# Kernel optimization log

Measured on AMD Instinct MI355X. Metric: run time of the kernel, lower is better.

## Reference

```python
import jax, jax.numpy as jnp
import numpy as np

FOCUS = 3  # focusing_factor
EPS = 1e-6


def setup_inputs() -> dict:
    key = jax.random.key(0)
    ks = jax.random.split(key, 6)
    B, N, C = 4, 4096, 1024
    s = 0.02
    return {
        "x": jax.random.normal(ks[0], (B, N, C), jnp.float32),
        "w_qkv": jax.random.normal(ks[1], (3 * C, C), jnp.float32) * s,
        "w_proj": jax.random.normal(ks[2], (C, C), jnp.float32) * s,
        "b_proj": jax.random.normal(ks[3], (C,), jnp.float32) * s,
        "w_dwc": jax.random.normal(ks[4], (C, 3), jnp.float32) * s,
        "b_dwc": jax.random.normal(ks[5], (C,), jnp.float32) * s,
    }


def _norm_last(t):
    return t / jnp.sum(t, axis=-1, keepdims=True)


def reference(x, w_qkv, w_proj, b_proj, w_dwc, b_dwc):
    B, N, C = x.shape
    H = 16
    d = C // H
    # qkv projection -> (3, B, H, N, d)
    qkv = jnp.einsum('bnc,oc->bno', x, w_qkv).reshape(B, N, 3, H, d)
    qkv = jnp.transpose(qkv, (2, 0, 3, 1, 4))
    q, k, v = qkv[0], qkv[1], qkv[2]
    # focused kernel feature map: relu -> l1 norm -> power -> renorm
    q = _norm_last(jax.nn.relu(q) + EPS)
    k = _norm_last(jax.nn.relu(k) + EPS)
    q = _norm_last(q ** FOCUS)
    k = _norm_last(k ** FOCUS)
    # linear attention
    kv = jnp.einsum('bhnd,bhne->bhde', k, v)                     # (B,H,d,d)
    z = 1.0 / (jnp.einsum('bhnd,bhd->bhn', q, k.sum(axis=2)) + EPS)
    out = jnp.einsum('bhnd,bhde,bhn->bhne', q, kv, z)            # (B,H,N,d)
    out = jnp.transpose(out, (0, 2, 1, 3)).reshape(B, N, C)
    # depthwise conv1d over sequence, kernel=3, padding=1 (torch layout [C,1,3])
    xp = jnp.pad(out, ((0, 0), (1, 1), (0, 0)))
    conv = (xp[:, 0:N, :] * w_dwc[:, 0]
            + xp[:, 1:N + 1, :] * w_dwc[:, 1]
            + xp[:, 2:N + 2, :] * w_dwc[:, 2]) + b_dwc
    out = out + conv
    # output projection (dropout is identity in eval)
    return jnp.einsum('bnc,oc->bno', out, w_proj) + b_proj
```

## Files before the change

kernel.cpp:

```cpp
#include <hip/hip_runtime.h>
#include <hip/hip_bf16.h>

#define BB 4
#define NN 4096
#define CC 1024
#define HH 16
#define MM (BB*NN)
#define EPSF 1e-6f

typedef _Float16 f16x8 __attribute__((ext_vector_type(8)));
typedef float f32x4 __attribute__((ext_vector_type(4)));

__device__ __forceinline__ void gload_lds16(const void* g, void* l) {
    __builtin_amdgcn_global_load_lds(
        (const __attribute__((address_space(1))) void*)g,
        (__attribute__((address_space(3))) void*)l, 16, 0, 0);
}

__device__ __forceinline__ float h2f(short s) {
    return (float)__builtin_bit_cast(_Float16, s);
}

__global__ __launch_bounds__(256)
void tofp16_kernel(const float* __restrict__ src, _Float16* __restrict__ dst, int n4)
{
    int i = blockIdx.x * 256 + threadIdx.x;
    if (i < n4) {
        float4 f = ((const float4*)src)[i];
        short4 pk;
        pk.x = __builtin_bit_cast(short, (_Float16)f.x);
        pk.y = __builtin_bit_cast(short, (_Float16)f.y);
        pk.z = __builtin_bit_cast(short, (_Float16)f.z);
        pk.w = __builtin_bit_cast(short, (_Float16)f.w);
        ((short4*)dst)[i] = pk;
    }
}


#define STAGE(BUF, KT) do {                                                          \
    _Pragma("unroll")                                                                \
    for (int j_ = 0; j_ < 2; ++j_) {                                                 \
        gload_lds16(gA[j_] + (KT) * 32, (char*)lds + (BUF) * 32768 + lbase[j_]);     \
        gload_lds16(gB[j_] + (KT) * 32, (char*)lds + (BUF) * 32768 + 16384 + lbase[j_]); \
    } } while (0)

#define TILE(KT, CUR, NXT, DOSTAGE, VMSTR) do {                                      \
    if (DOSTAGE) STAGE(NXT, (KT) + 2);                                               \
    const char* Ab_ = (const char*)lds + (CUR) * 32768 + aoff;                       \
    const char* Bb_ = (const char*)lds + (CUR) * 32768 + 16384 + boff;               \
    f16x8 af_[8], bf_[4];                                                            \
    _Pragma("unroll")                                                                \
    for (int m_ = 0; m_ < 8; ++m_) af_[m_] = *(const f16x8*)(Ab_ + m_ * 1024);       \
    _Pragma("unroll")                                                                \
    for (int n_ = 0; n_ < 4; ++n_) bf_[n_] = *(const f16x8*)(Bb_ + n_ * 1024);       \
    __builtin_amdgcn_s_setprio(1);                                                   \
    _Pragma("unroll")                                                                \
    for (int m_ = 0; m_ < 8; ++m_)                                                   \
    _Pragma("unroll")                                                                \
    for (int n_ = 0; n_ < 4; ++n_)                                                   \
        acc[m_][n_] = __builtin_amdgcn_mfma_f32_16x16x32_f16(af_[m_], bf_[n_],       \
                                                             acc[m_][n_], 0, 0, 0); \
    __builtin_amdgcn_s_setprio(0);                                                   \
    asm volatile("s_waitcnt " VMSTR ::: "memory");                                   \
    __builtin_amdgcn_s_barrier();                                                    \
    __builtin_amdgcn_sched_barrier(0);                                               \
} while (0)

template<int EPI>
__global__ __launch_bounds__(512, 2)
void gemm256(const _Float16* __restrict__ A, const _Float16* __restrict__ Bm,
             void* __restrict__ Cout, _Float16* __restrict__ Kt,
             _Float16* __restrict__ Vt, const float* __restrict__ bias,
             const int Ncols, const int gx)
{
    __shared__ _Float16 lds[3 * 16384];

    const int tid  = threadIdx.x;
    const int lane = tid & 63;
    const int wid  = tid >> 6;
    const int wm   = wid >> 2;
    const int wn   = wid & 3;

    const int nwg = gridDim.x;
    const int wg  = blockIdx.x;
    const int sw  = (wg & 7) * (nwg >> 3) + (wg >> 3);
    const int by  = sw / gx, bx = sw - by * gx;
    const int brow = by << 8, bcol = bx << 8;

    const _Float16* gA[2]; const _Float16* gB[2]; int lbase[2];
#pragma unroll
    for (int j = 0; j < 2; ++j) {
        int pos = ((wid * 2 + j) << 10) + (lane << 4);
        int r   = pos >> 6;
        int c8  = ((pos >> 4) & 3) ^ ((r >> 1) & 3);
        gA[j] = A  + (size_t)(brow + r) * 1024 + c8 * 8;
        gB[j] = Bm + (size_t)(bcol + r) * 1024 + c8 * 8;
        lbase[j] = (wid * 2 + j) << 10;
    }

    const int swz  = (((lane >> 4) ^ ((lane >> 1) & 3)) << 4);
    const int aoff = (wm * 128 + (lane & 15)) * 64 + swz;
    const int boff = (wn * 64  + (lane & 15)) * 64 + swz;

    f32x4 acc[8][4] = {};

    STAGE(0, 0);
    STAGE(1, 1);
    asm volatile("s_waitcnt vmcnt(4)" ::: "memory");
    __builtin_amdgcn_s_barrier();
    __builtin_amdgcn_sched_barrier(0);

#pragma unroll 1
    for (int tt = 0; tt < 30; tt += 3) {
        TILE(tt,     0, 2, 1, "vmcnt(4)");
        TILE(tt + 1, 1, 0, 1, "vmcnt(4)");
        TILE(tt + 2, 2, 1, 1, "vmcnt(4)");
    }
    TILE(30, 0, 2, 0, "vmcnt(0)");
    TILE(31, 1, 0, 0, "vmcnt(0)");

    if (EPI == 0) {
        const int sec = bcol >> 10;
        const bool feat = (sec < 2);
        if (feat) {
#pragma unroll
            for (int m = 0; m < 8; ++m)
#pragma unroll
                for (int r = 0; r < 4; ++r) {
                    float u[4]; float ssum = 0.f;
#pragma unroll
                    for (int n = 0; n < 4; ++n) {
                        float uu = fmaxf(acc[m][n][r], 0.f) + EPSF;
                        float c = uu * uu * uu;
                        u[n] = c; ssum += c;
                    }
                    ssum += __shfl_xor(ssum, 1, 16);
                    ssum += __shfl_xor(ssum, 2, 16);
                    ssum += __shfl_xor(ssum, 4, 16);
                    ssum += __shfl_xor(ssum, 8, 16);
                    float inv = 1.0f / ssum;
#pragma unroll
                    for (int n = 0; n < 4; ++n) acc[m][n][r] = u[n] * inv;
                }
        }
        if (sec == 0) {
            _Float16* Fo = (_Float16*)Cout;
            const int colb = bcol + wn * 64 + (lane & 15);
#pragma unroll
            for (int m = 0; m < 8; ++m) {
                int rb = brow + wm * 128 + m * 16 + (lane >> 4) * 4;
#pragma unroll
                for (int r = 0; r < 4; ++r) {
                    size_t base = (size_t)(rb + r) * 1024 + colb;
#pragma unroll
                    for (int n = 0; n < 4; ++n)
                        Fo[base + n * 16] = (_Float16)acc[m][n][r];
                }
            }
        } else {
            _Float16* T = (sec == 1) ? Kt : Vt;
            const int b   = brow >> 12;
            const int hb  = ((bcol & 1023) >> 6) + wn;
            const int bh  = b * 16 + hb;
            const int n0  = (brow & 4095) + wm * 128;
            char* st = (char*)lds + wid * 8704;
            const int p = lane & 15, q2 = lane >> 4;
#pragma unroll
            for (int c2 = 0; c2 < 2; ++c2) {
#pragma unroll
                for (int m = 0; m < 4; ++m) {
                    int mm = c2 * 4 + m;
                    int tokc = m * 16 + q2 * 4;
#pragma unroll
                    for (int n = 0; n < 4; ++n) {
                        short4 pk;
                        pk.x = __builtin_bit_cast(short, (_Float16)acc[mm][n][0]);
                        pk.y = __builtin_bit_cast(short, (_Float16)acc[mm][n][1]);
                        pk.z = __builtin_bit_cast(short, (_Float16)acc[mm][n][2]);
                        pk.w = __builtin_bit_cast(short, (_Float16)acc[mm][n][3]);
                        int dk = n * 16 + p;
                        *(short4*)(st + dk * 136 + tokc * 2) = pk;
                    }
                }
#pragma unroll
                for (int it = 0; it < 16; ++it) {
                    int dk = it * 4 + q2;
                    short4 v4 = *(const short4*)(st + dk * 136 + p * 8);
                    *(short4*)(T + ((size_t)(bh * 64 + dk)) * 4096 + n0 + c2 * 64 + p * 4) = v4;
                }
            }
        }
    } else {
        float* Oc = (float*)Cout;
        const int colb = bcol + wn * 64 + (lane & 15);
#pragma unroll
        for (int m = 0; m < 8; ++m) {
            int rb = brow + wm * 128 + m * 16 + (lane >> 4) * 4;
#pragma unroll
            for (int r = 0; r < 4; ++r) {
                size_t base = (size_t)(rb + r) * Ncols + colb;
#pragma unroll
                for (int n = 0; n < 4; ++n)
                    Oc[base + n * 16] = acc[m][n][r] + bias[colb + n * 16];
            }
        }
    }
}

__global__ __launch_bounds__(256)
void kv_mfma(const _Float16* __restrict__ Kt, const _Float16* __restrict__ Vt,
             float* __restrict__ kvp, float* __restrict__ ksump)
{
    __shared__ float red[4][64][64];
    __shared__ float ksr[4][64];
    int bx = blockIdx.x;
    int bh = bx >> 2, kseg = bx & 3;
    int tid = threadIdx.x;
    int w = tid >> 6, lane = tid & 63, p = lane & 15, q = lane >> 4;
    const _Float16* Vb = Vt + (size_t)bh * 64 * 4096;
    const _Float16* Kb = Kt + (size_t)bh * 64 * 4096;
    f32x4 acc[4][4] = {};
    float ksp[4] = {0.f, 0.f, 0.f, 0.f};
    int kbase = kseg * 1024 + w * 256 + q * 8;
#pragma unroll 1
    for (int ks = 0; ks < 8; ++ks) {
        int kb = kbase + ks * 32;
        f16x8 af[4], bf[4];
#pragma unroll
        for (int m = 0; m < 4; ++m)
            af[m] = *(const f16x8*)(Vb + (size_t)(m * 16 + p) * 4096 + kb);
#pragma unroll
        for (int n = 0; n < 4; ++n) {
            bf[n] = *(const f16x8*)(Kb + (size_t)(n * 16 + p) * 4096 + kb);
#pragma unroll
            for (int j = 0; j < 8; ++j) ksp[n] += (float)bf[n][j];
        }
#pragma unroll
        for (int m = 0; m < 4; ++m)
#pragma unroll
            for (int n = 0; n < 4; ++n)
                acc[m][n] = __builtin_amdgcn_mfma_f32_16x16x32_f16(
                    af[m], bf[n], acc[m][n], 0, 0, 0);
    }
#pragma unroll
    for (int n = 0; n < 4; ++n) {
        ksp[n] += __shfl_xor(ksp[n], 16);
        ksp[n] += __shfl_xor(ksp[n], 32);
    }
    if (q == 0)
#pragma unroll
        for (int n = 0; n < 4; ++n) ksr[w][n * 16 + p] = ksp[n];
#pragma unroll
    for (int m = 0; m < 4; ++m)
#pragma unroll
        for (int n = 0; n < 4; ++n)
            *(f32x4*)&red[w][n * 16 + p][m * 16 + q * 4] = acc[m][n];
    __syncthreads();
    int dv = tid & 63, dkb = (tid >> 6) * 16;
    float* ko = kvp + ((size_t)(kseg * 64 + bh)) * 4096;
    f32x4 o[4];
#pragma unroll
    for (int i = 0; i < 16; ++i) {
        float s = red[0][dkb + i][dv] + red[1][dkb + i][dv]
                + red[2][dkb + i][dv] + red[3][dkb + i][dv];
        o[i >> 2][i & 3] = s;
    }
#pragma unroll
    for (int i = 0; i < 4; ++i)
        *(f32x4*)(ko + dv * 64 + dkb + i * 4) = o[i];
    if (tid < 64)
        ksump[(size_t)(kseg * 64 + bh) * 64 + tid] =
            ksr[0][tid] + ksr[1][tid] + ksr[2][tid] + ksr[3][tid];
}

__global__ __launch_bounds__(256)
void kv_reduce(const float* __restrict__ kvp, const float* __restrict__ ksump,
               _Float16* __restrict__ kvT, float* __restrict__ ksum)
{
    int idx = blockIdx.x * 256 + threadIdx.x;
    float s = kvp[idx] + kvp[262144 + idx] + kvp[2 * 262144 + idx] + kvp[3 * 262144 + idx];
    kvT[idx] = (_Float16)s;
    if (idx < 4096)
        ksum[idx] = ksump[idx] + ksump[4096 + idx] + ksump[2 * 4096 + idx] + ksump[3 * 4096 + idx];
}

__global__ __launch_bounds__(256)
void attn_conv(const _Float16* __restrict__ Fq, const _Float16* __restrict__ kvT,
               const float* __restrict__ ksum, const float* __restrict__ wdwc,
               const float* __restrict__ bdwc, _Float16* __restrict__ yf)
{
    __shared__ _Float16 ybuf[258][68];
    __shared__ float kslds[64];
    int blk = blockIdx.x;
    int b = blk >> 8, h = (blk >> 4) & 15, chunk = blk & 15;
    int bh = b * 16 + h;
    int tid = threadIdx.x, w = tid >> 6, lane = tid & 63, p = lane & 15, q = lane >> 4;
    if (tid < 64) kslds[tid] = ksum[bh * 64 + tid];
    const _Float16* kvb = kvT + (size_t)bh * 4096;
    f16x8 bf[2][4];
#pragma unroll
    for (int kst = 0; kst < 2; ++kst)
#pragma unroll
        for (int n = 0; n < 4; ++n)
            bf[kst][n] = *(const f16x8*)(kvb + (n * 16 + p) * 64 + kst * 32 + q * 8);
    __syncthreads();

    int tok0 = chunk * 256 + w * 64;
    const size_t rowbase = (size_t)(b * 4096 + tok0);
    f16x8 qr[8];
#pragma unroll
    for (int i = 0; i < 8; ++i)
        qr[i] = *(const f16x8*)(Fq + (rowbase + lane) * 1024 + h * 64 + i * 8);
    float s = 0.f;
#pragma unroll
    for (int i = 0; i < 8; ++i)
#pragma unroll
        for (int j = 0; j < 8; ++j)
            s += (float)qr[i][j] * kslds[i * 8 + j];
    float z = 1.0f / (s + EPSF);

    f32x4 acc[4][4] = {};
#pragma unroll
    for (int kst = 0; kst < 2; ++kst) {
        f16x8 af[4];
#pragma unroll
        for (int m = 0; m < 4; ++m)
            af[m] = *(const f16x8*)(Fq + (rowbase + m * 16 + p) * 1024 + h * 64 + kst * 32 + q * 8);
#pragma unroll
        for (int m = 0; m < 4; ++m)
#pragma unroll
            for (int n = 0; n < 4; ++n)
                acc[m][n] = __builtin_amdgcn_mfma_f32_16x16x32_f16(
                    af[m], bf[kst][n], acc[m][n], 0, 0, 0);
    }
#pragma unroll
    for (int m = 0; m < 4; ++m)
#pragma unroll
        for (int r = 0; r < 4; ++r) {
            float zz = __shfl(z, m * 16 + q * 4 + r);
            int row = 1 + w * 64 + m * 16 + q * 4 + r;
#pragma unroll
            for (int n = 0; n < 4; ++n)
                ybuf[row][n * 16 + p] = (_Float16)(acc[m][n][r] * zz);
        }
    if (w == 0) {
        float val = 0.f;
        if (chunk > 0) {
            int t = chunk * 256 - 1;
            float sd = 0.f, sz = 0.f;
#pragma unroll
            for (int i = 0; i < 8; ++i) {
                f16x8 qq = *(const f16x8*)(Fq + ((size_t)(b * 4096 + t)) * 1024 + h * 64 + i * 8);
                f16x8 kk = *(const f16x8*)(kvb + lane * 64 + i * 8);
#pragma unroll
                for (int j = 0; j < 8; ++j) {
                    sd += (float)qq[j] * (float)kk[j];
                    sz += (float)qq[j] * kslds[i * 8 + j];
                }
            }
            val = sd / (sz + EPSF);
        }
        ybuf[0][lane] = (_Float16)val;
    }
    if (w == 3) {
        float val = 0.f;
        if (chunk < 15) {
            int t = chunk * 256 + 256;
            float sd = 0.f, sz = 0.f;
#pragma unroll
            for (int i = 0; i < 8; ++i) {
                f16x8 qq = *(const f16x8*)(Fq + ((size_t)(b * 4096 + t)) * 1024 + h * 64 + i * 8);
                f16x8 kk = *(const f16x8*)(kvb + lane * 64 + i * 8);
#pragma unroll
                for (int j = 0; j < 8; ++j) {
                    sd += (float)qq[j] * (float)kk[j];
                    sz += (float)qq[j] * kslds[i * 8 + j];
                }
            }
            val = sd / (sz + EPSF);
        }
        ybuf[257][lane] = (_Float16)val;
    }
    __syncthreads();
    int dv = lane;
    int c = h * 64 + dv;
    float w0 = wdwc[c * 3 + 0], w1 = wdwc[c * 3 + 1], w2 = wdwc[c * 3 + 2];
    float bb = bdwc[c];
#pragma unroll 4
    for (int it = 0; it < 64; ++it) {
        int tok = it * 4 + w;
        float ym = (float)ybuf[tok][dv];
        float yc = (float)ybuf[tok + 1][dv];
        float yp = (float)ybuf[tok + 2][dv];
        float val = yc + w0 * ym + w1 * yc + w2 * yp + bb;
        yf[((size_t)(b * 4096 + chunk * 256 + tok)) * 1024 + c] = (_Float16)val;
    }
}

extern "C" void kernel_launch(void* const* d_in, const int* in_sizes, int n_in,
                              void* d_out, int out_size, void* d_ws, size_t ws_size,
                              hipStream_t stream)
{
    const float* x      = (const float*)d_in[0];
    const float* w_qkv  = (const float*)d_in[1];
    const float* w_proj = (const float*)d_in[2];
    const float* b_proj = (const float*)d_in[3];
    const float* w_dwc  = (const float*)d_in[4];
    const float* b_dwc  = (const float*)d_in[5];

    char* p = (char*)d_ws;
    _Float16* xf   = (_Float16*)p;  p += (size_t)MM * CC * 2;
    _Float16* wqf  = (_Float16*)p;  p += (size_t)3 * CC * CC * 2;
    _Float16* wpf  = (_Float16*)p;  p += (size_t)CC * CC * 2;
    _Float16* Fq   = (_Float16*)p;  p += (size_t)MM * CC * 2;
    _Float16* Kt   = (_Float16*)p;  p += (size_t)64 * 64 * NN * 2;
    _Float16* Vt   = (_Float16*)p;  p += (size_t)64 * 64 * NN * 2;
    float*    kvp  = (float*)p;     p += (size_t)4 * 64 * 4096 * 4;
    float*    ksump= (float*)p;     p += (size_t)4 * 64 * 64 * 4;
    _Float16* kvT  = (_Float16*)p;  p += (size_t)64 * 4096 * 2;
    float*    ksum = (float*)p;     p += (size_t)64 * 64 * 4;
    _Float16* yf   = (_Float16*)p;  p += (size_t)MM * CC * 2;

    tofp16_kernel<<<(MM * CC / 4 + 255) / 256, 256, 0, stream>>>(x, xf, MM * CC / 4);
    tofp16_kernel<<<(3 * CC * CC / 4 + 255) / 256, 256, 0, stream>>>(w_qkv, wqf, 3 * CC * CC / 4);
    tofp16_kernel<<<(CC * CC / 4 + 255) / 256, 256, 0, stream>>>(w_proj, wpf, CC * CC / 4);

    gemm256<0><<<dim3(12 * 64), 512, 0, stream>>>(
        xf, wqf, (void*)Fq, Kt, Vt, nullptr, 3072, 12);

    kv_mfma<<<256, 256, 0, stream>>>(Kt, Vt, kvp, ksump);
    kv_reduce<<<1024, 256, 0, stream>>>(kvp, ksump, kvT, ksum);

    attn_conv<<<BB * HH * 16, 256, 0, stream>>>(Fq, kvT, ksum, w_dwc, b_dwc, yf);

    gemm256<1><<<dim3(4 * 64), 512, 0, stream>>>(
        yf, wpf, d_out, nullptr, nullptr, b_proj, 1024, 4);
}
```

Before: 224.2 us.

## Restructure GEMM main loop to K=64 double-buffered tiles with interleaved staging

The 256x256 fp16 GEMM main loop moves from a triple-buffered K=32 pipeline to a double-buffered K=64 tile with a new XOR swizzle for 128-byte rows. Each tile is split into four MFMA phases with barriers, and the global-to-LDS loads for the next tile are interleaved between phases. The goal is to halve loop iterations and barrier overhead per K step and to overlap LDS fragment reads and global loads with MFMA work. In exchange it needs more LDS (128KB per block, which may cut occupancy below the launch bound of 2) and adds more barriers within each tile.

```diff
diff --git a/kernel.cpp b/kernel.cpp
--- a/kernel.cpp
+++ b/kernel.cpp
@@ -37,34 +37,85 @@
 }
 
 
-#define STAGE(BUF, KT) do {                                                          \
-    _Pragma("unroll")                                                                \
-    for (int j_ = 0; j_ < 2; ++j_) {                                                 \
-        gload_lds16(gA[j_] + (KT) * 32, (char*)lds + (BUF) * 32768 + lbase[j_]);     \
-        gload_lds16(gB[j_] + (KT) * 32, (char*)lds + (BUF) * 32768 + 16384 + lbase[j_]); \
-    } } while (0)
-
-#define TILE(KT, CUR, NXT, DOSTAGE, VMSTR) do {                                      \
-    if (DOSTAGE) STAGE(NXT, (KT) + 2);                                               \
-    const char* Ab_ = (const char*)lds + (CUR) * 32768 + aoff;                       \
-    const char* Bb_ = (const char*)lds + (CUR) * 32768 + 16384 + boff;               \
-    f16x8 af_[8], bf_[4];                                                            \
-    _Pragma("unroll")                                                                \
-    for (int m_ = 0; m_ < 8; ++m_) af_[m_] = *(const f16x8*)(Ab_ + m_ * 1024);       \
-    _Pragma("unroll")                                                                \
-    for (int n_ = 0; n_ < 4; ++n_) bf_[n_] = *(const f16x8*)(Bb_ + n_ * 1024);       \
-    __builtin_amdgcn_s_setprio(1);                                                   \
-    _Pragma("unroll")                                                                \
-    for (int m_ = 0; m_ < 8; ++m_)                                                   \
-    _Pragma("unroll")                                                                \
-    for (int n_ = 0; n_ < 4; ++n_)                                                   \
-        acc[m_][n_] = __builtin_amdgcn_mfma_f32_16x16x32_f16(af_[m_], bf_[n_],       \
-                                                             acc[m_][n_], 0, 0, 0); \
-    __builtin_amdgcn_s_setprio(0);                                                   \
-    asm volatile("s_waitcnt " VMSTR ::: "memory");                                   \
-    __builtin_amdgcn_s_barrier();                                                    \
-    __builtin_amdgcn_sched_barrier(0);                                               \
-} while (0)
+#define BARX  do { __builtin_amdgcn_s_barrier(); __builtin_amdgcn_sched_barrier(0); } while(0)
+#define LGKM0 do { asm volatile("s_waitcnt lgkmcnt(0)" ::: "memory"); \
+                   __builtin_amdgcn_sched_barrier(0); } while(0)
+#define VMW8   asm volatile("s_waitcnt vmcnt(8)" ::: "memory")
+#define VMW0   asm volatile("s_waitcnt vmcnt(0)" ::: "memory")
+#define VMNONE ((void)0)
+
+#define STAGEA(H, CUR, TT) do {                                               \
+    _Pragma("unroll")                                                         \
+    for (int i_ = 2*(H); i_ < 2*(H)+2; ++i_)                                  \
+        gload_lds16(gA[i_] + (TT)*64,                                         \
+            (char*)lds + (CUR)*65536 + i_*8192 + tid*16);                     \
+} while(0)
+#define STAGEB(H, CUR, TT) do {                                               \
+    _Pragma("unroll")                                                         \
+    for (int i_ = 2*(H); i_ < 2*(H)+2; ++i_)                                  \
+        gload_lds16(gB[i_] + (TT)*64,                                         \
+            (char*)lds + (CUR)*65536 + 32768 + i_*8192 + tid*16);             \
+} while(0)
+
+#define TILE8(CUR, TT, STG, VMACT) do {                                       \
+    const char* bc_ = (const char*)lds + (CUR)*65536;                         \
+    f16x8 fb_[2][4], fa0_[2][2], fa1_[2][4], fa2_[2][2];                      \
+                               \
+    _Pragma("unroll") for (int kk_ = 0; kk_ < 2; ++kk_) {                     \
+        _Pragma("unroll") for (int n_ = 0; n_ < 4; ++n_)                      \
+            fb_[kk_][n_] = *(const f16x8*)(bc_ + boffk[kk_] + n_*2048);       \
+        _Pragma("unroll") for (int j_ = 0; j_ < 2; ++j_)                      \
+            fa0_[kk_][j_] = *(const f16x8*)(bc_ + aoffk[kk_] + j_*2048);      \
+    }                                                                         \
+    BARX; LGKM0;                                                              \
+    __builtin_amdgcn_s_setprio(1);                                            \
+    _Pragma("unroll") for (int kk_ = 0; kk_ < 2; ++kk_)                       \
+    _Pragma("unroll") for (int j_ = 0; j_ < 2; ++j_)                          \
+    _Pragma("unroll") for (int n_ = 0; n_ < 4; ++n_)                          \
+        acc[j_][n_] = __builtin_amdgcn_mfma_f32_16x16x32_f16(                 \
+            fa0_[kk_][j_], fb_[kk_][n_], acc[j_][n_], 0, 0, 0);               \
+    __builtin_amdgcn_s_setprio(0);                                            \
+    BARX;                                                                     \
+                        \
+    _Pragma("unroll") for (int kk_ = 0; kk_ < 2; ++kk_)                       \
+    _Pragma("unroll") for (int j_ = 0; j_ < 4; ++j_)                          \
+        fa1_[kk_][j_] = *(const f16x8*)(bc_ + aoffk[kk_] + (2+j_)*2048);      \
+    if (STG) STAGEB(0, CUR, (TT)+2);                                          \
+    BARX; LGKM0;                                                              \
+    __builtin_amdgcn_s_setprio(1);                                            \
+    _Pragma("unroll") for (int kk_ = 0; kk_ < 2; ++kk_)                       \
+    _Pragma("unroll") for (int j_ = 0; j_ < 2; ++j_)                          \
+    _Pragma("unroll") for (int n_ = 0; n_ < 4; ++n_)                          \
+        acc[2+j_][n_] = __builtin_amdgcn_mfma_f32_16x16x32_f16(               \
+            fa1_[kk_][j_], fb_[kk_][n_], acc[2+j_][n_], 0, 0, 0);             \
+    __builtin_amdgcn_s_setprio(0);                                            \
+    BARX;                                                                     \
+                                 \
+    _Pragma("unroll") for (int kk_ = 0; kk_ < 2; ++kk_)                       \
+    _Pragma("unroll") for (int j_ = 0; j_ < 2; ++j_)                          \
+        fa2_[kk_][j_] = *(const f16x8*)(bc_ + aoffk[kk_] + (6+j_)*2048);      \
+    __builtin_amdgcn_s_setprio(1);                                            \
+    _Pragma("unroll") for (int kk_ = 0; kk_ < 2; ++kk_)                       \
+    _Pragma("unroll") for (int j_ = 0; j_ < 2; ++j_)                          \
+    _Pragma("unroll") for (int n_ = 0; n_ < 4; ++n_)                          \
+        acc[4+j_][n_] = __builtin_amdgcn_mfma_f32_16x16x32_f16(               \
+            fa1_[kk_][2+j_], fb_[kk_][n_], acc[4+j_][n_], 0, 0, 0);           \
+    __builtin_amdgcn_s_setprio(0);                                            \
+    LGKM0;                                                                    \
+    BARX;                                                                     \
+                     \
+    if (STG) { STAGEA(0, CUR, (TT)+2); STAGEA(1, CUR, (TT)+2);                \
+               STAGEB(1, CUR, (TT)+2); }                                      \
+    __builtin_amdgcn_s_setprio(1);                                            \
+    _Pragma("unroll") for (int kk_ = 0; kk_ < 2; ++kk_)                       \
+    _Pragma("unroll") for (int j_ = 0; j_ < 2; ++j_)                          \
+    _Pragma("unroll") for (int n_ = 0; n_ < 4; ++n_)                          \
+        acc[6+j_][n_] = __builtin_amdgcn_mfma_f32_16x16x32_f16(               \
+            fa2_[kk_][j_], fb_[kk_][n_], acc[6+j_][n_], 0, 0, 0);             \
+    __builtin_amdgcn_s_setprio(0);                                            \
+    VMACT;                                                                    \
+    BARX;                                                                     \
+} while(0)
 
 template<int EPI>
 __global__ __launch_bounds__(512, 2)
@@ -73,7 +124,7 @@
              _Float16* __restrict__ Vt, const float* __restrict__ bias,
              const int Ncols, const int gx)
 {
-    __shared__ _Float16 lds[3 * 16384];
+    __shared__ _Float16 lds[2 * 32768];
 
     const int tid  = threadIdx.x;
     const int lane = tid & 63;
@@ -87,37 +138,40 @@
     const int by  = sw / gx, bx = sw - by * gx;
     const int brow = by << 8, bcol = bx << 8;
 
-    const _Float16* gA[2]; const _Float16* gB[2]; int lbase[2];
-#pragma unroll
-    for (int j = 0; j < 2; ++j) {
-        int pos = ((wid * 2 + j) << 10) + (lane << 4);
-        int r   = pos >> 6;
-        int c8  = ((pos >> 4) & 3) ^ ((r >> 1) & 3);
-        gA[j] = A  + (size_t)(brow + r) * 1024 + c8 * 8;
-        gB[j] = Bm + (size_t)(bcol + r) * 1024 + c8 * 8;
-        lbase[j] = (wid * 2 + j) << 10;
-    }
-
-    const int swz  = (((lane >> 4) ^ ((lane >> 1) & 3)) << 4);
-    const int aoff = (wm * 128 + (lane & 15)) * 64 + swz;
-    const int boff = (wn * 64  + (lane & 15)) * 64 + swz;
+    const int srow  = tid >> 3;
+    const int sclog = (tid & 7) ^ (srow & 7);
+    const _Float16* gA[4]; const _Float16* gB[4];
+#pragma unroll
+    for (int i = 0; i < 4; ++i) {
+        gA[i] = A  + (size_t)(brow + i * 64 + srow) * 1024 + sclog * 8;
+        gB[i] = Bm + (size_t)(bcol + i * 64 + srow) * 1024 + sclog * 8;
+    }
+
+    const int l15 = lane & 15, q = lane >> 4, s = l15 & 7;
+    const int chunkbase = ((q ^ (s & 3)) << 4) + (((s >> 2) & 1) << 6);
+    int aoffk[2], boffk[2];
+#pragma unroll
+    for (int kk = 0; kk < 2; ++kk) {
+        aoffk[kk] = (wm * 128 + l15) * 128 + (chunkbase ^ (kk << 6));
+        boffk[kk] = 32768 + (wn * 64 + l15) * 128 + (chunkbase ^ (kk << 6));
+    }
 
     f32x4 acc[8][4] = {};
 
-    STAGE(0, 0);
-    STAGE(1, 1);
-    asm volatile("s_waitcnt vmcnt(4)" ::: "memory");
-    __builtin_amdgcn_s_barrier();
-    __builtin_amdgcn_sched_barrier(0);
+    STAGEA(0, 0, 0); STAGEA(1, 0, 0); STAGEB(0, 0, 0); STAGEB(1, 0, 0);
+    STAGEA(0, 1, 1); STAGEA(1, 1, 1); STAGEB(0, 1, 1); STAGEB(1, 1, 1);
+    VMW8;
+    BARX;
 
 #pragma unroll 1
-    for (int tt = 0; tt < 30; tt += 3) {
-        TILE(tt,     0, 2, 1, "vmcnt(4)");
-        TILE(tt + 1, 1, 0, 1, "vmcnt(4)");
-        TILE(tt + 2, 2, 1, 1, "vmcnt(4)");
-    }
-    TILE(30, 0, 2, 0, "vmcnt(0)");
-    TILE(31, 1, 0, 0, "vmcnt(0)");
+    for (int tt = 0; tt < 12; tt += 2) {
+        TILE8(0, tt,     1, VMW8);
+        TILE8(1, tt + 1, 1, VMW8);
+    }
+    TILE8(0, 12, 1, VMW8);
+    TILE8(1, 13, 1, VMW8);
+    TILE8(0, 14, 0, VMW0);
+    TILE8(1, 15, 0, VMNONE);
 
     if (EPI == 0) {
         const int sec = bcol >> 10;
@@ -145,10 +199,10 @@
         }
         if (sec == 0) {
             _Float16* Fo = (_Float16*)Cout;
-            const int colb = bcol + wn * 64 + (lane & 15);
+            const int colb = bcol + wn * 64 + l15;
 #pragma unroll
             for (int m = 0; m < 8; ++m) {
-                int rb = brow + wm * 128 + m * 16 + (lane >> 4) * 4;
+                int rb = brow + wm * 128 + m * 16 + q * 4;
 #pragma unroll
                 for (int r = 0; r < 4; ++r) {
                     size_t base = (size_t)(rb + r) * 1024 + colb;
@@ -164,7 +218,7 @@
             const int bh  = b * 16 + hb;
             const int n0  = (brow & 4095) + wm * 128;
             char* st = (char*)lds + wid * 8704;
-            const int p = lane & 15, q2 = lane >> 4;
+            const int p = l15, q2 = q;
 #pragma unroll
             for (int c2 = 0; c2 < 2; ++c2) {
 #pragma unroll
@@ -192,10 +246,10 @@
         }
     } else {
         float* Oc = (float*)Cout;
-        const int colb = bcol + wn * 64 + (lane & 15);
+        const int colb = bcol + wn * 64 + l15;
 #pragma unroll
         for (int m = 0; m < 8; ++m) {
-            int rb = brow + wm * 128 + m * 16 + (lane >> 4) * 4;
+            int rb = brow + wm * 128 + m * 16 + q * 4;
 #pragma unroll
             for (int r = 0; r < 4; ++r) {
                 size_t base = (size_t)(rb + r) * Ncols + colb;
```

After: 230.4 us. +2.7%, slower.
